# Kernel tuning notes

Hardware: AMD Instinct MI355X
Metric: run time of the kernel (lower is better)

Reference implementation:

```python
import jax, jax.numpy as jnp
import numpy as np

N = 20000          # num nodes
E = 400000         # num edges
F_NODE = 16        # node_features
F_EDGE = 16        # edge_features
H = 128            # hidden_size
D = 16             # node_embedding_dim
DE = 16            # edge_embedding_dim


def setup_inputs() -> dict:
    key = jax.random.key(0)
    ks = jax.random.split(key, 16)
    s = 0.1
    inp = {
        "x": jax.random.normal(ks[0], (N, F_NODE), jnp.float32),
        "edge_index": jax.random.randint(ks[1], (2, E), 0, N, dtype=jnp.int64),
        "edge_attr": jax.random.normal(ks[2], (E, F_EDGE), jnp.float32),
        # node_embedding: Linear(F_NODE, D)
        "Wn": jax.random.normal(ks[3], (F_NODE, D), jnp.float32) * s,
        "bn": jnp.zeros((D,), jnp.float32),
        # edge_embedding: Linear(F_EDGE, DE)
        "We": jax.random.normal(ks[4], (F_EDGE, DE), jnp.float32) * s,
        "be": jnp.zeros((DE,), jnp.float32),
        # shared edge MLP: Linear(F_EDGE, H) -> ReLU -> Linear(H, 2*D*D)
        "W1": jax.random.normal(ks[5], (F_EDGE, H), jnp.float32) * s,
        "b1": jnp.zeros((H,), jnp.float32),
        "W2": jax.random.normal(ks[6], (H, 2 * D * D), jnp.float32) * s,
        "b2": jnp.zeros((2 * D * D,), jnp.float32),
        # per-layer root weights and biases
        "root1": jax.random.normal(ks[7], (D, D), jnp.float32) * s,
        "bias1": jnp.zeros((D,), jnp.float32),
        "root2": jax.random.normal(ks[8], (D, D), jnp.float32) * s,
        "bias2": jnp.zeros((D,), jnp.float32),
    }
    return inp


def _graph_conv(h, src, dst, edge_attr, W1, b1, W2, b2, root, bias):
    # per-edge weight from shared MLP: [E, 2D*D] -> [E, 2D, D]
    w = jnp.maximum(edge_attr @ W1 + b1, 0.0) @ W2 + b2
    w = w.reshape(E, 2 * D, D)
    # gather endpoint features; x_i = target, x_j = source (PyG flow)
    nf = jnp.concatenate([h[dst], h[src]], axis=1)           # [E, 2D]
    msg = jnp.einsum("ek,ekd->ed", nf, w)                    # [E, D]
    aggr = jax.ops.segment_sum(msg, dst, num_segments=N)     # [N, D]
    return aggr + h @ root + bias


def reference(x, edge_index, edge_attr, Wn, bn, We, be, W1, b1, W2, b2,
              root1, bias1, root2, bias2):
    src, dst = edge_index[0], edge_index[1]
    h = jnp.maximum(x @ Wn + bn, 0.0)                        # node embedding [N, D]
    h = _graph_conv(h, src, dst, edge_attr, W1, b1, W2, b2, root1, bias1)
    h = _graph_conv(h, src, dst, edge_attr, W1, b1, W2, b2, root2, bias2)
    ee = jnp.maximum(edge_attr @ We + be, 0.0)               # edge embedding [E, DE]
    return h, edge_index, ee, jax.nn.log_softmax(ee, axis=-1)
```

## Files before the change

### kernel.cpp

```cpp
#include <hip/hip_runtime.h>
#include <hip/hip_bf16.h>


#define NN 20000
#define NE 400000

typedef unsigned short u16;
typedef unsigned int   u32;
typedef __attribute__((ext_vector_type(8))) short short8;
typedef __attribute__((ext_vector_type(4))) float f32x4;

__device__ __forceinline__ float bf2f(u16 h) {
  union { u32 u; float f; } v; v.u = ((u32)h) << 16; return v.f;
}
__device__ __forceinline__ u16 f2bf(float f) {
  union { float f; u32 u; } v; v.f = f;
  return (u16)((v.u + 0x7FFFu + ((v.u >> 16) & 1u)) >> 16);
}
__device__ __forceinline__ float ldf(const void* p, size_t i, int f32m) {
  return f32m ? ((const float*)p)[i] : bf2f(((const u16*)p)[i]);
}
__device__ __forceinline__ int ldi(const void* p, size_t i, int i64m) {
  return i64m ? (int)((const long long*)p)[i] : ((const int*)p)[i];
}
__device__ __forceinline__ void stf(void* p, size_t i, float v, int f32m) {
  if (f32m) ((float*)p)[i] = v; else ((u16*)p)[i] = f2bf(v);
}

__global__ void k_detect(const u16* __restrict__ x16,
                         const int* __restrict__ ei32, int* __restrict__ flags) {
  int t = blockIdx.x * 256 + threadIdx.x;
  int found_f32 = 0, found_hi = 0;
  for (int i = t; i < NN * 16; i += 64 * 256) {
    u16 v = x16[i];
    if ((v & 0x7F80u) == 0x7F80u) found_f32 = 1;
  }
  for (int i = t; i < 200000; i += 64 * 256)
    if (ei32[2 * i + 1] != 0) found_hi = 1;
  if (__any(found_f32) && (threadIdx.x & 63) == 0) atomicOr(&flags[0], 1);
  if (__any(found_hi) && (threadIdx.x & 63) == 0) atomicOr(&flags[1], 1);
}

__global__ void k_pack_w2(const void* __restrict__ W2, u16* __restrict__ w2p,
                          const int* __restrict__ flags) {
  const int f32m = flags[0];
  int t = blockIdx.x * 256 + threadIdx.x;
  if (t >= 32 * 4 * 64) return;
  int lane = t & 63;
  int ks = (t >> 6) & 3;
  int kb = t >> 8;
  int n = lane & 15, q = lane >> 4;
  for (int j = 0; j < 8; ++j) {
    int h = ks * 32 + q * 8 + j;
    w2p[(size_t)t * 8 + j] = f2bf(ldf(W2, (size_t)h * 512 + kb * 16 + n, f32m));
  }
}

__global__ void k_pack_w1(const void* __restrict__ W1, u16* __restrict__ w1p,
                          const int* __restrict__ flags) {
  const int f32m = flags[0];
  int t = blockIdx.x * 256 + threadIdx.x;
  if (t >= 8 * 64) return;
  int lane = t & 63;
  int n = t >> 6;
  int col = n * 16 + (lane & 15), q = lane >> 4;
  for (int j = 0; j < 8; ++j) {
    int kk = q * 8 + j;
    w1p[(size_t)t * 8 + j] = (kk < 16) ? f2bf(ldf(W1, (size_t)kk * 128 + col, f32m)) : (u16)0;
  }
}

__global__ void k_pack_qd(const void* __restrict__ W2, u16* __restrict__ w2q,
                          u16* __restrict__ w2d, const int* __restrict__ flags) {
  const int f32m = flags[0];
  int t = blockIdx.x * 256 + threadIdx.x;
  if (t >= 8192) return;
  int lane = t & 63, q = lane >> 4, l16 = lane & 15;
  if (t < 4096) {
    int kc = t >> 6;
#pragma unroll
    for (int jj = 0; jj < 8; ++jj) {
      int kj = kc * 32 + q * 8 + jj;
      int j = kj >> 4, ks = kj & 15;
      w2q[(size_t)t * 8 + jj] =
          f2bf(ldf(W2, (size_t)j * 512 + (16 + ks) * 16 + l16, f32m));
    }
  } else {
    int u = t - 4096;
    int ct = u >> 8;
    int jc = (u >> 6) & 3;
#pragma unroll
    for (int jj = 0; jj < 8; ++jj) {
      int j = jc * 32 + q * 8 + jj;
      w2d[(size_t)u * 8 + jj] =
          f2bf(ldf(W2, (size_t)j * 512 + ct * 16 + l16, f32m));
    }
  }
}

__global__ void k_embed(const void* __restrict__ x, const void* __restrict__ Wn,
                        const void* __restrict__ bn, float* __restrict__ h0,
                        const int* __restrict__ flags) {
  const int f32m = flags[0];
  int t = blockIdx.x * 256 + threadIdx.x;
  if (t >= NN * 16) return;
  int n = t >> 4, d = t & 15;
  float acc = ldf(bn, d, f32m);
  for (int k = 0; k < 16; ++k)
    acc += ldf(x, n * 16 + k, f32m) * ldf(Wn, k * 16 + d, f32m);
  h0[t] = fmaxf(acc, 0.f);
}

__global__ void k_count(const void* __restrict__ ei, int* __restrict__ cnt,
                        const int* __restrict__ flags) {
  const int i64m = !flags[1];
  int i = blockIdx.x * 256 + threadIdx.x;
  if (i < NE) atomicAdd(&cnt[ldi(ei, NE + i, i64m)], 1);
}

__global__ void k_scan(const int* __restrict__ cnt, int* __restrict__ rowptr,
                       int* __restrict__ cursor) {
  __shared__ int part[1024];
  int t = threadIdx.x;
  int base = t * 20;
  int s = 0;
  for (int j = 0; j < 20; ++j) { int idx = base + j; if (idx < NN) s += cnt[idx]; }
  part[t] = s;
  __syncthreads();
  for (int off = 1; off < 1024; off <<= 1) {
    int v = (t >= off) ? part[t - off] : 0;
    __syncthreads();
    part[t] += v;
    __syncthreads();
  }
  int run = t ? part[t - 1] : 0;
  for (int j = 0; j < 20; ++j) {
    int idx = base + j;
    if (idx < NN) {
      int c = cnt[idx];
      rowptr[idx] = run; cursor[idx] = run; run += c;
    }
  }
  if (t == 1023) rowptr[NN] = part[1023];
}

__global__ void k_scatter(const void* __restrict__ ei, int* __restrict__ cursor,
                          int* __restrict__ inv, int* __restrict__ srcp,
                          int* __restrict__ eperm, const int* __restrict__ flags) {
  const int i64m = !flags[1];
  int i = blockIdx.x * 256 + threadIdx.x;
  if (i >= NE) return;
  int d = ldi(ei, NE + i, i64m);
  int pos = atomicAdd(&cursor[d], 1);
  if (inv)   inv[i] = pos;
  if (srcp)  srcp[pos] = ldi(ei, i, i64m);
  if (eperm) eperm[pos] = i;
}

__global__ void k_eap(const void* __restrict__ ea, const int* __restrict__ eperm,
                      u16* __restrict__ eap, const int* __restrict__ flags) {
  const int f32m = flags[0];
  int t = blockIdx.x * 256 + threadIdx.x;
  if (t >= NE) return;
  int e = eperm[t];
  union { uint4 q[2]; u16 h[16]; } o;
  if (f32m) {
    const float4* ep = (const float4*)((const float*)ea + (size_t)e * 16);
    float4 a = ep[0], b = ep[1], c = ep[2], d = ep[3];
    o.h[0]=f2bf(a.x);  o.h[1]=f2bf(a.y);  o.h[2]=f2bf(a.z);  o.h[3]=f2bf(a.w);
    o.h[4]=f2bf(b.x);  o.h[5]=f2bf(b.y);  o.h[6]=f2bf(b.z);  o.h[7]=f2bf(b.w);
    o.h[8]=f2bf(c.x);  o.h[9]=f2bf(c.y);  o.h[10]=f2bf(c.z); o.h[11]=f2bf(c.w);
    o.h[12]=f2bf(d.x); o.h[13]=f2bf(d.y); o.h[14]=f2bf(d.z); o.h[15]=f2bf(d.w);
  } else {
    const uint4* ep = (const uint4*)((const u16*)ea + (size_t)e * 16);
    o.q[0] = ep[0]; o.q[1] = ep[1];
  }
  uint4* dp = (uint4*)(eap + (size_t)t * 16);
  dp[0] = o.q[0]; dp[1] = o.q[1];
}

__launch_bounds__(256)
__attribute__((amdgpu_waves_per_eu(2, 4)))
__global__ void k_node(const int* __restrict__ rowptr,
                       const int* __restrict__ srcperm,
                       const u16* __restrict__ eap,
                       const float* __restrict__ hin,
                       const u16* __restrict__ w1p,
                       const void* __restrict__ b1,
                       const u16* __restrict__ w2q,
                       const u16* __restrict__ w2d,
                       const void* __restrict__ b2,
                       const void* __restrict__ root,
                       const void* __restrict__ bias,
                       float* __restrict__ hout, void* __restrict__ out,
                       const int* __restrict__ flags) {
  __shared__ u16   T_lds[4 * 2048];
  __shared__ u32   S_lds[4 * 64];
  __shared__ float hs_lds[4 * 16];
  __shared__ float h_lds[4 * 16];
  __shared__ float part_lds[4 * 256];
  __shared__ float b1_lds[128];
  __shared__ u16   w1_lds[4096];
  __shared__ u32   BB_lds[4][320];
  const int f32m = flags[0];
  const int t = threadIdx.x;
  const int lane = t & 63, w = t >> 6;
  const int q = lane >> 4, l16 = lane & 15;
  const int n0 = blockIdx.x * 4;
  const short8 z8 = {0,0,0,0,0,0,0,0};

  if (t < 64) h_lds[t] = hin[(size_t)(n0 + (t >> 4)) * 16 + (t & 15)];
  if (t < 128) b1_lds[t] = ldf(b1, t, f32m);
  {
    const uint4* src = (const uint4*)w1p;
    uint4* dst = (uint4*)w1_lds;
    dst[t] = src[t];
    dst[t + 256] = src[t + 256];
  }

  short8 ONES;
  { union { u32 u[4]; short8 s; } o;
    o.u[0] = 0x3F803F80u; o.u[1] = 0x3F803F80u;
    o.u[2] = 0x3F803F80u; o.u[3] = 0x3F803F80u; ONES = o.s; }

  __syncthreads();

  const int nb = w;
  {
    const int n  = n0 + nb;
    const int beg = rowptr[n], end = rowptr[n + 1];

    f32x4 accT[8];
    float S8[8];
    f32x4 accH = {0.f, 0.f, 0.f, 0.f};
#pragma unroll
    for (int c = 0; c < 8; ++c) {
      accT[c][0] = 0.f; accT[c][1] = 0.f; accT[c][2] = 0.f; accT[c][3] = 0.f;
      S8[c] = 0.f;
    }

    for (int g = (beg & ~31); g < end; g += 32) {
      int src_l = (lane < 32) ? srcperm[g + lane] : 0;
      union { u32 u[4]; short8 s; } Ahi, Alo, Amk;
#pragma unroll
      for (int jp = 0; jp < 4; ++jp) {
        const int k0 = q * 8 + 2 * jp, k1 = k0 + 1;
        int s0 = __shfl(src_l, k0);
        int s1 = __shfl(src_l, k1);
        float h0 = hin[(size_t)s0 * 16 + l16];
        float h1 = hin[(size_t)s1 * 16 + l16];
        const int v0 = (g + k0 >= beg) && (g + k0 < end);
        const int v1 = (g + k1 >= beg) && (g + k1 < end);
        h0 = v0 ? h0 : 0.f;
        h1 = v1 ? h1 : 0.f;
        union { float f; u32 u; } b0, b1u; b0.f = h0; b1u.f = h1;
        u32 hi0 = b0.u >> 16, hi1 = b1u.u >> 16;
        union { u32 u; float f; } r0, r1; r0.u = hi0 << 16; r1.u = hi1 << 16;
        u32 lo0 = f2bf(h0 - r0.f), lo1 = f2bf(h1 - r1.f);
        Ahi.u[jp] = hi0 | (hi1 << 16);
        Alo.u[jp] = lo0 | (lo1 << 16);
        Amk.u[jp] = (v0 ? 0x3F80u : 0u) | (v1 ? 0x3F800000u : 0u);
      }

      short8 ea0 = z8, ea1 = z8;
      if (q < 2) {
        ea0 = *(const short8*)(eap + (size_t)(g + l16) * 16 + q * 8);
        ea1 = *(const short8*)(eap + (size_t)(g + 16 + l16) * 16 + q * 8);
      }

#pragma unroll
      for (int c = 0; c < 8; ++c) {
        short8 Wf = *(const short8*)&w1_lds[c * 512 + lane * 8];
        f32x4 ca = {0.f, 0.f, 0.f, 0.f}, cb = {0.f, 0.f, 0.f, 0.f};
        ca = __builtin_amdgcn_mfma_f32_16x16x32_bf16(ea0, Wf, ca, 0, 0, 0);
        cb = __builtin_amdgcn_mfma_f32_16x16x32_bf16(ea1, Wf, cb, 0, 0, 0);
        float bb = b1_lds[c * 16 + l16];
        u32 p00 = (u32)f2bf(fmaxf(ca[0] + bb, 0.f)) |
                  ((u32)f2bf(fmaxf(ca[1] + bb, 0.f)) << 16);
        u32 p01 = (u32)f2bf(fmaxf(ca[2] + bb, 0.f)) |
                  ((u32)f2bf(fmaxf(ca[3] + bb, 0.f)) << 16);
        u32 p10 = (u32)f2bf(fmaxf(cb[0] + bb, 0.f)) |
                  ((u32)f2bf(fmaxf(cb[1] + bb, 0.f)) << 16);
        u32 p11 = (u32)f2bf(fmaxf(cb[2] + bb, 0.f)) |
                  ((u32)f2bf(fmaxf(cb[3] + bb, 0.f)) << 16);
        u32* bw = &BB_lds[w][l16 * 20];
        uint2 w0; w0.x = p00; w0.y = p01;
        uint2 w1v; w1v.x = p10; w1v.y = p11;
        *(uint2*)&bw[q * 2]     = w0;
        *(uint2*)&bw[8 + q * 2] = w1v;
        short8 Bf = *(const short8*)&bw[q * 4];
        accT[c] = __builtin_amdgcn_mfma_f32_16x16x32_bf16(Ahi.s, Bf, accT[c], 0, 0, 0);
        accT[c] = __builtin_amdgcn_mfma_f32_16x16x32_bf16(Alo.s, Bf, accT[c], 0, 0, 0);
        f32x4 cs = {0.f, 0.f, 0.f, 0.f};
        cs = __builtin_amdgcn_mfma_f32_16x16x32_bf16(Amk.s, Bf, cs, 0, 0, 0);
        S8[c] += cs[0];
      }
      accH = __builtin_amdgcn_mfma_f32_16x16x32_bf16(Ahi.s, ONES, accH, 0, 0, 0);
      accH = __builtin_amdgcn_mfma_f32_16x16x32_bf16(Alo.s, ONES, accH, 0, 0, 0);
    }

    {
      char* Tl = (char*)T_lds;
#pragma unroll
      for (int c = 0; c < 8; ++c) {
        u32 p0 = (u32)f2bf(accT[c][0]) | ((u32)f2bf(accT[c][1]) << 16);
        u32 p1 = (u32)f2bf(accT[c][2]) | ((u32)f2bf(accT[c][3]) << 16);
        int b   = (c * 16 + l16) * 32 + q * 8;
        int key = ((nb ^ (c * 8 + (l16 >> 1))) & 7) << 4;
        uint2 pv; pv.x = p0; pv.y = p1;
        *(uint2*)(Tl + (size_t)nb * 4096 + (b ^ key)) = pv;
      }
      if (q == 0) {
        u16* s16 = (u16*)S_lds;
#pragma unroll
        for (int c = 0; c < 8; ++c)
          s16[nb * 128 + c * 16 + l16] = f2bf(S8[c]);
      }
      if (l16 == 0) *(f32x4*)&hs_lds[nb * 16 + q * 4] = accH;
    }
  }
  __syncthreads();

  const int row = l16;
  f32x4 c1 = {0.f, 0.f, 0.f, 0.f};
  {
    const short8* w2qf = (const short8*)w2q;
#pragma unroll
    for (int kk = 0; kk < 16; ++kk) {
      int kc = w * 16 + kk;
      int off = ((row & 3) * 4096 + kc * 64 + q * 16) ^ ((((row ^ kc) & 7)) << 4);
      short8 af = *(const short8*)((const char*)T_lds + off);
      if (row >= 4) af = z8;
      short8 bf = w2qf[kc * 64 + lane];
      c1 = __builtin_amdgcn_mfma_f32_16x16x32_bf16(af, bf, c1, 0, 0, 0);
    }
  }
  f32x4 c2_0 = {0,0,0,0}, c2_1 = {0,0,0,0}, c2_2 = {0,0,0,0}, c2_3 = {0,0,0,0};
  {
    short8 as0, as1, as2, as3;
    {
      const u32* sb = S_lds + (row & 3) * 64 + q * 4;
      as0 = *(const short8*)(sb + 0);
      as1 = *(const short8*)(sb + 16);
      as2 = *(const short8*)(sb + 32);
      as3 = *(const short8*)(sb + 48);
      if (row >= 4) { as0 = z8; as1 = z8; as2 = z8; as3 = z8; }
    }
    const short8* w2df = (const short8*)w2d;
#pragma unroll
    for (int ci = 0; ci < 4; ++ci) {
      int ct = w * 4 + ci;
      f32x4 cc = {0.f, 0.f, 0.f, 0.f};
      cc = __builtin_amdgcn_mfma_f32_16x16x32_bf16(as0, w2df[(ct * 4 + 0) * 64 + lane], cc, 0, 0, 0);
      cc = __builtin_amdgcn_mfma_f32_16x16x32_bf16(as1, w2df[(ct * 4 + 1) * 64 + lane], cc, 0, 0, 0);
      cc = __builtin_amdgcn_mfma_f32_16x16x32_bf16(as2, w2df[(ct * 4 + 2) * 64 + lane], cc, 0, 0, 0);
      cc = __builtin_amdgcn_mfma_f32_16x16x32_bf16(as3, w2df[(ct * 4 + 3) * 64 + lane], cc, 0, 0, 0);
      if (ci == 0) c2_0 = cc; else if (ci == 1) c2_1 = cc;
      else if (ci == 2) c2_2 = cc; else c2_3 = cc;
    }
  }
#pragma unroll
  for (int r = 0; r < 4; ++r) {
    int nrow = q * 4 + r;
    const float* hp = h_lds + (nrow & 3) * 16 + w * 4;
    float a = c1[r];
    a += hp[0] * c2_0[r];
    a += hp[1] * c2_1[r];
    a += hp[2] * c2_2[r];
    a += hp[3] * c2_3[r];
    part_lds[w * 256 + nrow * 16 + l16] = a;
  }
  __syncthreads();

  if (t < 64) {
    int nb2 = t >> 4, d = t & 15;
    int n = n0 + nb2;
    float acc = part_lds[nb2 * 16 + d] + part_lds[256 + nb2 * 16 + d] +
                part_lds[512 + nb2 * 16 + d] + part_lds[768 + nb2 * 16 + d];
    float dg = (float)(rowptr[n + 1] - rowptr[n]);
    acc += ldf(bias, d, f32m);
#pragma unroll
    for (int k = 0; k < 16; ++k) {
      float hv = h_lds[nb2 * 16 + k];
      acc += hv * (ldf(root, (size_t)k * 16 + d, f32m) +
                   dg * ldf(b2, (size_t)k * 16 + d, f32m));
      acc += hs_lds[nb2 * 16 + k] * ldf(b2, (size_t)256 + k * 16 + d, f32m);
    }
    if (hout) hout[(size_t)n * 16 + d] = acc;
    else      stf(out, (size_t)n * 16 + d, acc, f32m);
  }
}

__launch_bounds__(256, 2)
__global__ void k_edge(const void* __restrict__ ea, const void* __restrict__ ei,
                       const float* __restrict__ hprev,
                       const u16* __restrict__ w2p, const u16* __restrict__ w1p,
                       const void* __restrict__ b1, const void* __restrict__ b2,
                       u16* __restrict__ msg16, float* __restrict__ aggr,
                       const int* __restrict__ inv,
                       const int* __restrict__ flags, int use_csr) {
  __shared__ u16   a2_lds[128 * 136];
  __shared__ float nfT[32 * 132];
  __shared__ float msg_lds[128 * 17];
  __shared__ float b1_lds[128];
  __shared__ int   dst_lds[128];

  const int f32m = flags[0], i64m = !flags[1];
  const int t = threadIdx.x;
  const int lane = t & 63, w = t >> 6;
  const int q = lane >> 4, l16 = lane & 15;
  const int e0 = blockIdx.x * 128;

  short8 B[8][4];
  {
    const short8* w2pf = (const short8*)w2p;
#pragma unroll
    for (int i = 0; i < 8; ++i)
#pragma unroll
      for (int ks = 0; ks < 4; ++ks)
        B[i][ks] = w2pf[((w * 8 + i) * 4 + ks) * 64 + lane];
  }
  float b2v[8];
#pragma unroll
  for (int i = 0; i < 8; ++i) b2v[i] = ldf(b2, (w * 8 + i) * 16 + l16, f32m);
  short8 W1f[8];
  {
    const short8* w1pf = (const short8*)w1p;
#pragma unroll
    for (int n = 0; n < 8; ++n) W1f[n] = w1pf[n * 64 + lane];
  }
  if (t < 128) b1_lds[t] = ldf(b1, t, f32m);

  {
    int e = t >> 1, hh = t & 1;
    int node = hh ? ldi(ei, e0 + e, i64m) : ldi(ei, NE + e0 + e, i64m);
    const float4* hp = (const float4*)(hprev + (size_t)node * 16);
    float4 h0v = hp[0], h1v = hp[1], h2v = hp[2], h3v = hp[3];
    float* col = nfT + (size_t)(hh * 16) * 132 + e;
    col[0 * 132] = h0v.x; col[1 * 132] = h0v.y; col[2 * 132] = h0v.z; col[3 * 132] = h0v.w;
    col[4 * 132] = h1v.x; col[5 * 132] = h1v.y; col[6 * 132] = h1v.z; col[7 * 132] = h1v.w;
    col[8 * 132] = h2v.x; col[9 * 132] = h2v.y; col[10 * 132] = h2v.z; col[11 * 132] = h2v.w;
    col[12 * 132] = h3v.x; col[13 * 132] = h3v.y; col[14 * 132] = h3v.z; col[15 * 132] = h3v.w;
    if (!hh) {
      if (use_csr) dst_lds[e] = inv[e0 + e];
      else         dst_lds[e] = node;
    }
    float* mz = msg_lds + e * 17 + hh * 8;
#pragma unroll
    for (int k2 = 0; k2 < 8; ++k2) mz[k2] = 0.f;
  }
  __syncthreads();

#pragma unroll
  for (int mm = 0; mm < 2; ++mm) {
    int m = w * 2 + mm;
    union { short8 s; u16 h[8]; } ua;
    if (q < 2) {
      if (f32m) {
        const float* er = (const float*)ea + ((size_t)(e0 + m * 16 + l16) * 16 + q * 8);
        float4 f0 = *(const float4*)er;
        float4 f1 = *(const float4*)(er + 4);
        ua.h[0] = f2bf(f0.x); ua.h[1] = f2bf(f0.y); ua.h[2] = f2bf(f0.z); ua.h[3] = f2bf(f0.w);
        ua.h[4] = f2bf(f1.x); ua.h[5] = f2bf(f1.y); ua.h[6] = f2bf(f1.z); ua.h[7] = f2bf(f1.w);
      } else {
        ua.s = *(const short8*)((const u16*)ea + ((size_t)(e0 + m * 16 + l16) * 16 + q * 8));
      }
    } else {
#pragma unroll
      for (int j = 0; j < 8; ++j) ua.h[j] = 0;
    }
    short8 A = ua.s;
#pragma unroll
    for (int n = 0; n < 8; ++n) {
      f32x4 c = {0.f, 0.f, 0.f, 0.f};
      c = __builtin_amdgcn_mfma_f32_16x16x32_bf16(A, W1f[n], c, 0, 0, 0);
      float bb = b1_lds[n * 16 + l16];
#pragma unroll
      for (int r = 0; r < 4; ++r)
        a2_lds[(m * 16 + q * 4 + r) * 136 + n * 16 + l16] =
            f2bf(fmaxf(c[r] + bb, 0.f));
    }
  }
  __syncthreads();

#pragma unroll 1
  for (int mi = 0; mi < 8; ++mi) {
    int m = (mi + w * 2) & 7;
    const short8* ap = (const short8*)&a2_lds[(m * 16 + l16) * 136 + q * 8];
    short8 A0 = ap[0], A1 = ap[4], A2f = ap[8], A3 = ap[12];
    float mr0 = 0.f, mr1 = 0.f, mr2 = 0.f, mr3 = 0.f;
#pragma unroll
    for (int i = 0; i < 8; ++i) {
      f32x4 c = {b2v[i], b2v[i], b2v[i], b2v[i]};
      c = __builtin_amdgcn_mfma_f32_16x16x32_bf16(A0, B[i][0], c, 0, 0, 0);
      c = __builtin_amdgcn_mfma_f32_16x16x32_bf16(A1, B[i][1], c, 0, 0, 0);
      c = __builtin_amdgcn_mfma_f32_16x16x32_bf16(A2f, B[i][2], c, 0, 0, 0);
      c = __builtin_amdgcn_mfma_f32_16x16x32_bf16(A3, B[i][3], c, 0, 0, 0);
      int kb = w * 8 + i;
      f32x4 nf4 = *(const f32x4*)&nfT[(size_t)kb * 132 + m * 16 + q * 4];
      mr0 += nf4[0] * c[0];
      mr1 += nf4[1] * c[1];
      mr2 += nf4[2] * c[2];
      mr3 += nf4[3] * c[3];
    }
    int eb = (m * 16 + q * 4) * 17 + l16;
    atomicAdd(&msg_lds[eb + 0 * 17], mr0);
    atomicAdd(&msg_lds[eb + 1 * 17], mr1);
    atomicAdd(&msg_lds[eb + 2 * 17], mr2);
    atomicAdd(&msg_lds[eb + 3 * 17], mr3);
  }
  __syncthreads();

  {
    int e = t >> 1, dh = t & 1;
    const float* mp = msg_lds + e * 17 + dh * 8;
    if (use_csr) {
      int pos = dst_lds[e];
      union { uint4 qv; u16 h[8]; } pk;
#pragma unroll
      for (int dd = 0; dd < 8; ++dd) pk.h[dd] = f2bf(mp[dd]);
      *(uint4*)(msg16 + (size_t)pos * 16 + dh * 8) = pk.qv;
    } else {
      int dnode = dst_lds[e];
      float* ap2 = aggr + (size_t)dnode * 16 + dh * 8;
#pragma unroll
      for (int dd = 0; dd < 8; ++dd) atomicAdd(ap2 + dd, mp[dd]);
    }
  }
}

__global__ void k_gather(const u16* __restrict__ msg16,
                         const int* __restrict__ rowptr,
                         const float* __restrict__ h_old,
                         const void* __restrict__ root,
                         const void* __restrict__ bias,
                         float* __restrict__ h_new, void* __restrict__ out,
                         const int* __restrict__ flags) {
  const int f32m = flags[0];
  __shared__ float R[256];
  __shared__ float Bv[16];
  int tt = threadIdx.x;
  R[tt] = ldf(root, tt, f32m);
  if (tt < 16) Bv[tt] = ldf(bias, tt, f32m);
  __syncthreads();
  int t = blockIdx.x * 256 + tt;
  if (t >= NN * 16) return;
  int n = t >> 4, d = t & 15;
  float acc = Bv[d];
#pragma unroll
  for (int k = 0; k < 16; ++k) acc += h_old[n * 16 + k] * R[k * 16 + d];
  int beg = rowptr[n], end = rowptr[n + 1];
  for (int i = beg; i < end; ++i)
    acc += bf2f(msg16[(size_t)i * 16 + d]);
  if (h_new) h_new[t] = acc;
  else       stf(out, t, acc, f32m);
}

__global__ void k_combine(const float* __restrict__ h_old,
                          const float* __restrict__ aggr,
                          const void* __restrict__ root,
                          const void* __restrict__ bias,
                          float* __restrict__ h_new, void* __restrict__ out,
                          const int* __restrict__ flags) {
  const int f32m = flags[0];
  int t = blockIdx.x * 256 + threadIdx.x;
  if (t >= NN * 16) return;
  int n = t >> 4, d = t & 15;
  float acc = aggr[t] + ldf(bias, d, f32m);
  for (int k = 0; k < 16; ++k)
    acc += h_old[n * 16 + k] * ldf(root, (size_t)k * 16 + d, f32m);
  if (h_new) h_new[t] = acc;
  else       stf(out, t, acc, f32m);
}

__global__ void k_ee(const void* __restrict__ ea, const void* __restrict__ We,
                     const void* __restrict__ be, void* __restrict__ out,
                     const int* __restrict__ flags) {
  const int f32m = flags[0];
  __shared__ float W[256];
  __shared__ float Bv[16];
  int t = threadIdx.x;
  W[t] = ldf(We, t, f32m);
  if (t < 16) Bv[t] = ldf(be, t, f32m);
  __syncthreads();
  int e = blockIdx.x * 256 + t;
  if (e >= NE) return;
  float v[16];
  if (f32m) {
    const float4* ep = (const float4*)((const float*)ea + (size_t)e * 16);
    float4 r0 = ep[0], r1 = ep[1], r2 = ep[2], r3 = ep[3];
    v[0]=r0.x; v[1]=r0.y; v[2]=r0.z; v[3]=r0.w;
    v[4]=r1.x; v[5]=r1.y; v[6]=r1.z; v[7]=r1.w;
    v[8]=r2.x; v[9]=r2.y; v[10]=r2.z; v[11]=r2.w;
    v[12]=r3.x; v[13]=r3.y; v[14]=r3.z; v[15]=r3.w;
  } else {
    union { uint4 qv[2]; u16 h[16]; } rw;
    const uint4* ep = (const uint4*)((const u16*)ea + (size_t)e * 16);
    rw.qv[0] = ep[0]; rw.qv[1] = ep[1];
#pragma unroll
    for (int k = 0; k < 16; ++k) v[k] = bf2f(rw.h[k]);
  }
  float o[16];
  float mx = 0.f;
#pragma unroll
  for (int d = 0; d < 16; ++d) {
    float acc = Bv[d];
#pragma unroll
    for (int k = 0; k < 16; ++k) acc += v[k] * W[k * 16 + d];
    acc = fmaxf(acc, 0.f);
    o[d] = acc;
    mx = fmaxf(mx, acc);
  }
  float s = 0.f;
#pragma unroll
  for (int d = 0; d < 16; ++d) s += __expf(o[d] - mx);
  float lse = mx + __logf(s);
  const size_t off_ee = 1120000, off_ls = 7520000;
  if (f32m) {
    union { float4 fv; float f[4]; } pe, pl;
    float* oe = (float*)out + off_ee + (size_t)e * 16;
    float* ol = (float*)out + off_ls + (size_t)e * 16;
#pragma unroll
    for (int g = 0; g < 4; ++g) {
#pragma unroll
      for (int d = 0; d < 4; ++d) { pe.f[d] = o[g*4+d]; pl.f[d] = o[g*4+d] - lse; }
      ((float4*)oe)[g] = pe.fv;
      ((float4*)ol)[g] = pl.fv;
    }
  } else {
    union { uint4 qv[2]; u16 h[16]; } pe, pl;
#pragma unroll
    for (int d = 0; d < 16; ++d) {
      pe.h[d] = f2bf(o[d]);
      pl.h[d] = f2bf(o[d] - lse);
    }
    uint4* oe = (uint4*)((u16*)out + off_ee + (size_t)e * 16);
    uint4* ol = (uint4*)((u16*)out + off_ls + (size_t)e * 16);
    oe[0] = pe.qv[0]; oe[1] = pe.qv[1];
    ol[0] = pl.qv[0]; ol[1] = pl.qv[1];
  }
}

__global__ void k_idx(const void* __restrict__ ei, void* __restrict__ out,
                      const int* __restrict__ flags) {
  const int f32m = flags[0], i64m = !flags[1];
  int i = blockIdx.x * 256 + threadIdx.x;
  if (i >= 2 * NE) return;
  float v = i64m ? (float)((const long long*)ei)[i] : (float)((const int*)ei)[i];
  stf(out, (size_t)320000 + i, v, f32m);
}

extern "C" void kernel_launch(void* const* d_in, const int* in_sizes, int n_in,
                              void* d_out, int out_size, void* d_ws, size_t ws_size,
                              hipStream_t stream) {
  const void* x     = d_in[0];
  const void* ei    = d_in[1];
  const void* ea    = d_in[2];
  const void* Wn    = d_in[3];
  const void* bn    = d_in[4];
  const void* We    = d_in[5];
  const void* be    = d_in[6];
  const void* W1    = d_in[7];
  const void* b1    = d_in[8];
  const void* W2    = d_in[9];
  const void* b2    = d_in[10];
  const void* root1 = d_in[11];
  const void* bias1 = d_in[12];
  const void* root2 = d_in[13];
  const void* bias2 = d_in[14];

  char* ws = (char*)d_ws;
  const size_t need_new = 18859296;

  if (ws_size >= need_new) {
    int*   flags   = (int*)ws;
    float* h0      = (float*)(ws + 16);
    float* h1      = (float*)(ws + 1280016);
    u16*   w1p     = (u16*)(ws + 2560016);
    u16*   w2q     = (u16*)(ws + 2568208);
    u16*   w2d     = (u16*)(ws + 2633744);
    int*   rowptr  = (int*)(ws + 2699280);
    int*   cursor  = (int*)(ws + 2779296);
    int*   eperm   = (int*)(ws + 2859296);
    int*   srcperm = (int*)(ws + 4459296);
    u16*   eap     = (u16*)(ws + 6059296);

    hipMemsetAsync(flags, 0, 16, stream);
    k_detect<<<64, 256, 0, stream>>>((const u16*)x, (const int*)ei, flags);
    k_pack_w1<<<2, 256, 0, stream>>>(W1, w1p, flags);
    k_pack_qd<<<32, 256, 0, stream>>>(W2, w2q, w2d, flags);
    k_embed<<<1250, 256, 0, stream>>>(x, Wn, bn, h0, flags);

    hipMemsetAsync(cursor, 0, NN * 4, stream);
    k_count<<<1563, 256, 0, stream>>>(ei, cursor, flags);
    k_scan<<<1, 1024, 0, stream>>>(cursor, rowptr, cursor);
    k_scatter<<<1563, 256, 0, stream>>>(ei, cursor, nullptr, srcperm, eperm, flags);
    k_eap<<<1563, 256, 0, stream>>>(ea, eperm, eap, flags);

    k_node<<<5000, 256, 0, stream>>>(rowptr, srcperm, eap, h0, w1p, b1, w2q, w2d,
                                     b2, root1, bias1, h1, nullptr, flags);
    k_node<<<5000, 256, 0, stream>>>(rowptr, srcperm, eap, h1, w1p, b1, w2q, w2d,
                                     b2, root2, bias2, nullptr, d_out, flags);

    k_ee<<<1563, 256, 0, stream>>>(ea, We, be, d_out, flags);
    k_idx<<<3125, 256, 0, stream>>>(ei, d_out, flags);
    return;
  }

  int*   flags  = (int*)ws;
  float* h0     = (float*)(ws + 16);
  float* h1     = (float*)(ws + 1280016);
  u16*   w2p    = (u16*)(ws + 2560016);
  u16*   w1p    = (u16*)(ws + 2691088);
  u16*   msg16  = (u16*)(ws + 2699280);
  int*   rowptr = (int*)(ws + 15499280);
  int*   cursor = (int*)(ws + 15579296);
  int*   inv    = (int*)(ws + 15659296);
  const size_t need_csr = 17259296;
  float* aggr = (float*)(ws + 2699280);
  const int use_csr = (ws_size >= need_csr) ? 1 : 0;

  hipMemsetAsync(flags, 0, 16, stream);
  k_detect<<<64, 256, 0, stream>>>((const u16*)x, (const int*)ei, flags);
  k_pack_w2<<<32, 256, 0, stream>>>(W2, w2p, flags);
  k_pack_w1<<<2, 256, 0, stream>>>(W1, w1p, flags);
  k_embed<<<1250, 256, 0, stream>>>(x, Wn, bn, h0, flags);

  if (use_csr) {
    hipMemsetAsync(cursor, 0, NN * 4, stream);
    k_count<<<1563, 256, 0, stream>>>(ei, cursor, flags);
    k_scan<<<1, 1024, 0, stream>>>(cursor, rowptr, cursor);
    k_scatter<<<1563, 256, 0, stream>>>(ei, cursor, inv, nullptr, nullptr, flags);

    k_edge<<<3125, 256, 0, stream>>>(ea, ei, h0, w2p, w1p, b1, b2, msg16, nullptr, inv, flags, 1);
    k_gather<<<1250, 256, 0, stream>>>(msg16, rowptr, h0, root1, bias1, h1, nullptr, flags);
    k_edge<<<3125, 256, 0, stream>>>(ea, ei, h1, w2p, w1p, b1, b2, msg16, nullptr, inv, flags, 1);
    k_gather<<<1250, 256, 0, stream>>>(msg16, rowptr, h1, root2, bias2, nullptr, d_out, flags);
  } else {
    hipMemsetAsync(aggr, 0, (size_t)NN * 16 * 4, stream);
    k_edge<<<3125, 256, 0, stream>>>(ea, ei, h0, w2p, w1p, b1, b2, nullptr, aggr, nullptr, flags, 0);
    k_combine<<<1250, 256, 0, stream>>>(h0, aggr, root1, bias1, h1, nullptr, flags);
    hipMemsetAsync(aggr, 0, (size_t)NN * 16 * 4, stream);
    k_edge<<<3125, 256, 0, stream>>>(ea, ei, h1, w2p, w1p, b1, b2, nullptr, aggr, nullptr, flags, 0);
    k_combine<<<1250, 256, 0, stream>>>(h1, aggr, root2, bias2, nullptr, d_out, flags);
  }

  k_ee<<<1563, 256, 0, stream>>>(ea, We, be, d_out, flags);
  k_idx<<<3125, 256, 0, stream>>>(ei, d_out, flags);
}
```

Before: 402.3 us.

## Pad CSR rows to 32-edge groups and fuse edge-attr packing into scatter

Result: faster. 370.0 us (-8.0%).

```diff
diff --git a/kernel.cpp b/kernel.cpp
--- a/kernel.cpp
+++ b/kernel.cpp
@@ -144,44 +144,68 @@
   if (t == 1023) rowptr[NN] = part[1023];
 }
 
+__global__ void k_scanp(const int* __restrict__ deg, int* __restrict__ prow,
+                        int* __restrict__ cursor) {
+  __shared__ int part[1024];
+  int t = threadIdx.x;
+  int base = t * 20;
+  int s = 0;
+  for (int j = 0; j < 20; ++j) {
+    int idx = base + j;
+    if (idx < NN) s += (deg[idx] + 31) & ~31;
+  }
+  part[t] = s;
+  __syncthreads();
+  for (int off = 1; off < 1024; off <<= 1) {
+    int v = (t >= off) ? part[t - off] : 0;
+    __syncthreads();
+    part[t] += v;
+    __syncthreads();
+  }
+  int run = t ? part[t - 1] : 0;
+  for (int j = 0; j < 20; ++j) {
+    int idx = base + j;
+    if (idx < NN) {
+      int p = (deg[idx] + 31) & ~31;
+      prow[idx] = run; cursor[idx] = run; run += p;
+    }
+  }
+  if (t == 1023) prow[NN] = part[1023];
+}
+
 __global__ void k_scatter(const void* __restrict__ ei, int* __restrict__ cursor,
                           int* __restrict__ inv, int* __restrict__ srcp,
-                          int* __restrict__ eperm, const int* __restrict__ flags) {
-  const int i64m = !flags[1];
+                          const void* __restrict__ ea, u16* __restrict__ eap,
+                          const int* __restrict__ flags) {
+  const int f32m = flags[0], i64m = !flags[1];
   int i = blockIdx.x * 256 + threadIdx.x;
   if (i >= NE) return;
   int d = ldi(ei, NE + i, i64m);
   int pos = atomicAdd(&cursor[d], 1);
   if (inv)   inv[i] = pos;
   if (srcp)  srcp[pos] = ldi(ei, i, i64m);
-  if (eperm) eperm[pos] = i;
-}
-
-__global__ void k_eap(const void* __restrict__ ea, const int* __restrict__ eperm,
-                      u16* __restrict__ eap, const int* __restrict__ flags) {
-  const int f32m = flags[0];
-  int t = blockIdx.x * 256 + threadIdx.x;
-  if (t >= NE) return;
-  int e = eperm[t];
-  union { uint4 q[2]; u16 h[16]; } o;
-  if (f32m) {
-    const float4* ep = (const float4*)((const float*)ea + (size_t)e * 16);
-    float4 a = ep[0], b = ep[1], c = ep[2], d = ep[3];
-    o.h[0]=f2bf(a.x);  o.h[1]=f2bf(a.y);  o.h[2]=f2bf(a.z);  o.h[3]=f2bf(a.w);
-    o.h[4]=f2bf(b.x);  o.h[5]=f2bf(b.y);  o.h[6]=f2bf(b.z);  o.h[7]=f2bf(b.w);
-    o.h[8]=f2bf(c.x);  o.h[9]=f2bf(c.y);  o.h[10]=f2bf(c.z); o.h[11]=f2bf(c.w);
-    o.h[12]=f2bf(d.x); o.h[13]=f2bf(d.y); o.h[14]=f2bf(d.z); o.h[15]=f2bf(d.w);
-  } else {
-    const uint4* ep = (const uint4*)((const u16*)ea + (size_t)e * 16);
-    o.q[0] = ep[0]; o.q[1] = ep[1];
-  }
-  uint4* dp = (uint4*)(eap + (size_t)t * 16);
-  dp[0] = o.q[0]; dp[1] = o.q[1];
+  if (eap) {
+    union { uint4 q[2]; u16 h[16]; } o;
+    if (f32m) {
+      const float4* ep = (const float4*)((const float*)ea + (size_t)i * 16);
+      float4 a = ep[0], b = ep[1], c = ep[2], e4 = ep[3];
+      o.h[0]=f2bf(a.x);  o.h[1]=f2bf(a.y);  o.h[2]=f2bf(a.z);  o.h[3]=f2bf(a.w);
+      o.h[4]=f2bf(b.x);  o.h[5]=f2bf(b.y);  o.h[6]=f2bf(b.z);  o.h[7]=f2bf(b.w);
+      o.h[8]=f2bf(c.x);  o.h[9]=f2bf(c.y);  o.h[10]=f2bf(c.z); o.h[11]=f2bf(c.w);
+      o.h[12]=f2bf(e4.x); o.h[13]=f2bf(e4.y); o.h[14]=f2bf(e4.z); o.h[15]=f2bf(e4.w);
+    } else {
+      const uint4* ep = (const uint4*)((const u16*)ea + (size_t)i * 16);
+      o.q[0] = ep[0]; o.q[1] = ep[1];
+    }
+    uint4* dp = (uint4*)(eap + (size_t)pos * 16);
+    dp[0] = o.q[0]; dp[1] = o.q[1];
+  }
 }
 
 __launch_bounds__(256)
 __attribute__((amdgpu_waves_per_eu(2, 4)))
-__global__ void k_node(const int* __restrict__ rowptr,
+__global__ void k_node(const int* __restrict__ prow,
+                       const int* __restrict__ deg,
                        const int* __restrict__ srcperm,
                        const u16* __restrict__ eap,
                        const float* __restrict__ hin,
@@ -228,7 +252,8 @@
   const int nb = w;
   {
     const int n  = n0 + nb;
-    const int beg = rowptr[n], end = rowptr[n + 1];
+    const int beg = prow[n];
+    const int end = beg + deg[n];
 
     f32x4 accT[8];
     float S8[8];
@@ -239,7 +264,7 @@
       S8[c] = 0.f;
     }
 
-    for (int g = (beg & ~31); g < end; g += 32) {
+    for (int g = beg; g < end; g += 32) {
       int src_l = (lane < 32) ? srcperm[g + lane] : 0;
       union { u32 u[4]; short8 s; } Ahi, Alo, Amk;
 #pragma unroll
@@ -249,8 +274,8 @@
         int s1 = __shfl(src_l, k1);
         float h0 = hin[(size_t)s0 * 16 + l16];
         float h1 = hin[(size_t)s1 * 16 + l16];
-        const int v0 = (g + k0 >= beg) && (g + k0 < end);
-        const int v1 = (g + k1 >= beg) && (g + k1 < end);
+        const int v0 = (g + k0 < end);
+        const int v1 = (g + k1 < end);
         h0 = v0 ? h0 : 0.f;
         h1 = v1 ? h1 : 0.f;
         union { float f; u32 u; } b0, b1u; b0.f = h0; b1u.f = h1;
@@ -377,7 +402,7 @@
     int n = n0 + nb2;
     float acc = part_lds[nb2 * 16 + d] + part_lds[256 + nb2 * 16 + d] +
                 part_lds[512 + nb2 * 16 + d] + part_lds[768 + nb2 * 16 + d];
-    float dg = (float)(rowptr[n + 1] - rowptr[n]);
+    float dg = (float)deg[n];
     acc += ldf(bias, d, f32m);
 #pragma unroll
     for (int k = 0; k < 16; ++k) {
@@ -670,7 +695,7 @@
   const void* bias2 = d_in[14];
 
   char* ws = (char*)d_ws;
-  const size_t need_new = 18859296;
+  const size_t need_new = 39659296;
 
   if (ws_size >= need_new) {
     int*   flags   = (int*)ws;
@@ -679,27 +704,27 @@
     u16*   w1p     = (u16*)(ws + 2560016);
     u16*   w2q     = (u16*)(ws + 2568208);
     u16*   w2d     = (u16*)(ws + 2633744);
-    int*   rowptr  = (int*)(ws + 2699280);
-    int*   cursor  = (int*)(ws + 2779296);
-    int*   eperm   = (int*)(ws + 2859296);
-    int*   srcperm = (int*)(ws + 4459296);
-    u16*   eap     = (u16*)(ws + 6059296);
+    int*   deg     = (int*)(ws + 2699280);
+    int*   prow    = (int*)(ws + 2779280);
+    int*   cursor  = (int*)(ws + 2859296);
+    int*   srcperm = (int*)(ws + 2939296);
+    u16*   eap     = (u16*)(ws + 7019296);
 
     hipMemsetAsync(flags, 0, 16, stream);
+    hipMemsetAsync(deg, 0, 80000, stream);
+    hipMemsetAsync(srcperm, 0, 36720000, stream);
     k_detect<<<64, 256, 0, stream>>>((const u16*)x, (const int*)ei, flags);
     k_pack_w1<<<2, 256, 0, stream>>>(W1, w1p, flags);
     k_pack_qd<<<32, 256, 0, stream>>>(W2, w2q, w2d, flags);
     k_embed<<<1250, 256, 0, stream>>>(x, Wn, bn, h0, flags);
 
-    hipMemsetAsync(cursor, 0, NN * 4, stream);
-    k_count<<<1563, 256, 0, stream>>>(ei, cursor, flags);
-    k_scan<<<1, 1024, 0, stream>>>(cursor, rowptr, cursor);
-    k_scatter<<<1563, 256, 0, stream>>>(ei, cursor, nullptr, srcperm, eperm, flags);
-    k_eap<<<1563, 256, 0, stream>>>(ea, eperm, eap, flags);
-
-    k_node<<<5000, 256, 0, stream>>>(rowptr, srcperm, eap, h0, w1p, b1, w2q, w2d,
+    k_count<<<1563, 256, 0, stream>>>(ei, deg, flags);
+    k_scanp<<<1, 1024, 0, stream>>>(deg, prow, cursor);
+    k_scatter<<<1563, 256, 0, stream>>>(ei, cursor, nullptr, srcperm, ea, eap, flags);
+
+    k_node<<<5000, 256, 0, stream>>>(prow, deg, srcperm, eap, h0, w1p, b1, w2q, w2d,
                                      b2, root1, bias1, h1, nullptr, flags);
-    k_node<<<5000, 256, 0, stream>>>(rowptr, srcperm, eap, h1, w1p, b1, w2q, w2d,
+    k_node<<<5000, 256, 0, stream>>>(prow, deg, srcperm, eap, h1, w1p, b1, w2q, w2d,
                                      b2, root2, bias2, nullptr, d_out, flags);
 
     k_ee<<<1563, 256, 0, stream>>>(ea, We, be, d_out, flags);
@@ -730,7 +755,7 @@
     hipMemsetAsync(cursor, 0, NN * 4, stream);
     k_count<<<1563, 256, 0, stream>>>(ei, cursor, flags);
     k_scan<<<1, 1024, 0, stream>>>(cursor, rowptr, cursor);
-    k_scatter<<<1563, 256, 0, stream>>>(ei, cursor, inv, nullptr, nullptr, flags);
+    k_scatter<<<1563, 256, 0, stream>>>(ei, cursor, inv, nullptr, nullptr, nullptr, flags);
 
     k_edge<<<3125, 256, 0, stream>>>(ea, ei, h0, w2p, w1p, b1, b2, msg16, nullptr, inv, flags, 1);
     k_gather<<<1250, 256, 0, stream>>>(msg16, rowptr, h0, root1, bias1, h1, nullptr, flags);
```
